# Performance work log

Hardware: AMD Instinct MI355X
Metric: run time of the kernel (lower is better)

Reference implementation:

```python
import jax, jax.numpy as jnp
import numpy as np

NUM_USERS, NUM_ITEMS, NUM_GROUPS = 100000, 50000, 20000
D = 64
B, M = 16384, 50


def setup_inputs() -> dict:
    key = jax.random.key(0)
    ks = jax.random.split(key, 16)
    inp = {
        "group_inputs": jax.random.randint(ks[0], (B,), 0, NUM_GROUPS),
        "item_inputs": jax.random.randint(ks[1], (B,), 0, NUM_ITEMS),
        "member_ids": jax.random.randint(ks[2], (B, M), 0, NUM_USERS),
        "member_lengths": jax.random.randint(ks[3], (B,), 0, M),
        # embedding tables (xavier-ish scale)
        "user_table": jax.random.normal(ks[4], (NUM_USERS, D), jnp.float32) * 0.05,
        "item_table": jax.random.normal(ks[5], (NUM_ITEMS, D), jnp.float32) * 0.05,
        "group_table": jax.random.normal(ks[6], (NUM_GROUPS, D), jnp.float32) * 0.05,
        # attention MLP: 2D -> 16 -> 1
        "att_w1": jax.random.normal(ks[7], (2 * D, 16), jnp.float32) * 0.1,
        "att_b1": jnp.zeros((16,), jnp.float32),
        "att_w2": jax.random.normal(ks[8], (16, 1), jnp.float32) * 0.1,
        "att_b2": jnp.zeros((1,), jnp.float32),
        # predict MLP: 3D -> 8 -> 1
        "pred_w1": jax.random.normal(ks[9], (3 * D, 8), jnp.float32) * 0.1,
        "pred_b1": jnp.zeros((8,), jnp.float32),
        "pred_w2": jax.random.normal(ks[10], (8, 1), jnp.float32) * 0.1,
        "pred_b2": jnp.zeros((1,), jnp.float32),
    }
    return inp


def reference(group_inputs, item_inputs, member_ids, member_lengths,
              user_table, item_table, group_table,
              att_w1, att_b1, att_w2, att_b2,
              pred_w1, pred_b1, pred_w2, pred_b2):
    # mask: at least one valid member per group
    mask = jnp.arange(M)[None, :] <= member_lengths[:, None]          # [B, M] bool
    mem_e = user_table[member_ids]                                    # [B, M, D]
    item_e = item_table[item_inputs]                                  # [B, D]

    # attention over members: concat(member, item) -> 16 -> 1
    gi = jnp.concatenate(
        [mem_e, jnp.broadcast_to(item_e[:, None, :], mem_e.shape)], axis=-1)  # [B, M, 2D]
    h = jax.nn.relu(jnp.einsum('bmk,kh->bmh', gi, att_w1) + att_b1)   # [B, M, 16]
    scores = (jnp.einsum('bmh,ho->bmo', h, att_w2) + att_b2)[..., 0]  # [B, M]
    scores = jnp.where(mask, scores, -jnp.inf)
    at_wt = jax.nn.softmax(scores, axis=-1)                           # [B, M]

    g_att = jnp.einsum('bm,bmd->bd', at_wt, mem_e)                    # [B, D]
    g = g_att + group_table[group_inputs]                             # [B, D]

    elem = g * item_e
    new_e = jnp.concatenate([elem, g, item_e], axis=-1)               # [B, 3D]
    ph = jax.nn.relu(new_e @ pred_w1 + pred_b1)                       # [B, 8]
    y = jax.nn.sigmoid(ph @ pred_w2 + pred_b2)                        # [B, 1]
    return y
```

## Files before the change

kernel.cpp:

```cpp
#include <hip/hip_runtime.h>
#include <math.h>

constexpr int MM = 50;
constexpr int DD = 64;
constexpr int HH = 16;
constexpr int PH = 8;
constexpr int WAVES_PER_BLOCK = 4;
constexpr int SLOTS  = 56;
constexpr int CHUNKS = 7;

__device__ __forceinline__ unsigned bf16rne(float f) {
    const unsigned u = __float_as_uint(f);
    return (u + 0x7FFFu + ((u >> 16) & 1u)) >> 16;
}

__global__ __launch_bounds__(256) void precompute_kernel(
    const float* __restrict__ user_table,
    const float* __restrict__ item_table,
    const int*   __restrict__ item_inputs,
    const float* __restrict__ att_w1,
    const float* __restrict__ att_b1,
    unsigned short* __restrict__ Ubf,
    float* __restrict__ Ib,
    unsigned short* __restrict__ Ub,
    int nU, int B, int userBlocks)
{
    const bool isU = (int)blockIdx.x < userBlocks;
    const float4* rp;
    const float*  w1;
    float acc[HH];
    int row = 0;

    if (isU) {
        row = (int)blockIdx.x * 256 + (int)threadIdx.x;
        if (row >= nU) return;
        rp  = (const float4*)(user_table + (size_t)row * DD);
        w1  = att_w1;
        #pragma unroll
        for (int j = 0; j < HH; ++j) acc[j] = 0.0f;
    } else {
        row = ((int)blockIdx.x - userBlocks) * 256 + (int)threadIdx.x;
        if (row >= B) return;
        const int item = item_inputs[row];
        rp  = (const float4*)(item_table + (size_t)item * DD);
        w1  = att_w1 + (size_t)DD * HH;
        #pragma unroll
        for (int j = 0; j < HH; ++j) acc[j] = att_b1[j];
    }

    unsigned brow[DD / 2];

    #pragma unroll 4
    for (int d4 = 0; d4 < DD / 4; ++d4) {
        const float4 x = rp[d4];
        const float* w = w1 + (size_t)(d4 * 4) * HH;
        #pragma unroll
        for (int j = 0; j < HH; ++j) {
            acc[j] = fmaf(x.x, w[0 * HH + j], acc[j]);
            acc[j] = fmaf(x.y, w[1 * HH + j], acc[j]);
            acc[j] = fmaf(x.z, w[2 * HH + j], acc[j]);
            acc[j] = fmaf(x.w, w[3 * HH + j], acc[j]);
        }
        brow[2 * d4]     = bf16rne(x.x) | (bf16rne(x.y) << 16);
        brow[2 * d4 + 1] = bf16rne(x.z) | (bf16rne(x.w) << 16);
    }

    if (isU) {
        unsigned uw[8];
        #pragma unroll
        for (int w = 0; w < 8; ++w)
            uw[w] = bf16rne(acc[2 * w]) | (bf16rne(acc[2 * w + 1]) << 16);
        uint4* u4 = (uint4*)(Ubf + (size_t)row * HH);
        u4[0] = make_uint4(uw[0], uw[1], uw[2], uw[3]);
        u4[1] = make_uint4(uw[4], uw[5], uw[6], uw[7]);

        uint4* b4 = (uint4*)(Ub + (size_t)row * DD);
        #pragma unroll
        for (int i = 0; i < DD / 8; ++i)
            b4[i] = make_uint4(brow[4 * i], brow[4 * i + 1],
                               brow[4 * i + 2], brow[4 * i + 3]);
    } else {
        float4* o4 = (float4*)(Ib + (size_t)row * HH);
        o4[0] = make_float4(acc[0],  acc[1],  acc[2],  acc[3]);
        o4[1] = make_float4(acc[4],  acc[5],  acc[6],  acc[7]);
        o4[2] = make_float4(acc[8],  acc[9],  acc[10], acc[11]);
        o4[3] = make_float4(acc[12], acc[13], acc[14], acc[15]);
    }
}

__global__ __launch_bounds__(256) void agree_main(
    const int* __restrict__ group_inputs,
    const int* __restrict__ item_inputs,
    const int* __restrict__ member_ids,
    const int* __restrict__ member_lengths,
    const float* __restrict__ item_table,
    const float* __restrict__ group_table,
    const float* __restrict__ att_w2,
    const float* __restrict__ att_b2,
    const float* __restrict__ pred_w1,
    const float* __restrict__ pred_b1,
    const float* __restrict__ pred_w2,
    const float* __restrict__ pred_b2,
    const unsigned short* __restrict__ Ubf,
    const float* __restrict__ Ib,
    const unsigned short* __restrict__ Ub,
    float* __restrict__ out,
    int B)
{
    __shared__ float2 pairs[WAVES_PER_BLOCK][SLOTS];
    __shared__ float  gbuf[WAVES_PER_BLOCK][DD];

    const int lane = threadIdx.x & 63;
    const int wv   = threadIdx.x >> 6;
    const int b    = blockIdx.x * WAVES_PER_BLOCK + wv;
    if (b >= B) return;

    const int my_m  = (lane < MM) ? lane : (MM - 1);
    const int my_id = member_ids[b * MM + my_m];
    const int len      = member_lengths[b];
    const int item_idx = item_inputs[b];
    const int gid      = group_inputs[b];

    const float item_d = item_table[(unsigned)(item_idx * DD + lane)];
    const float grp_d  = group_table[(unsigned)(gid * DD + lane)];

    const uint4* up = (const uint4*)(Ubf + ((size_t)(unsigned)my_id * HH));
    const uint4 ua = up[0], ubw = up[1];
    const float* ib = Ib + (size_t)b * HH;

    float score = att_b2[0];
    {
        const unsigned uw[8] = { ua.x, ua.y, ua.z, ua.w,
                                 ubw.x, ubw.y, ubw.z, ubw.w };
        #pragma unroll
        for (int w = 0; w < 8; ++w) {
            const float f0 = __uint_as_float(uw[w] << 16);
            const float f1 = __uint_as_float(uw[w] & 0xFFFF0000u);
            score = fmaf(fmaxf(f0 + ib[2 * w],     0.0f), att_w2[2 * w],     score);
            score = fmaf(fmaxf(f1 + ib[2 * w + 1], 0.0f), att_w2[2 * w + 1], score);
        }
    }

    const bool valid = (lane < MM) && (lane <= len);
    score = valid ? score : -INFINITY;

    float mx = score;
    #pragma unroll
    for (int off = 32; off > 0; off >>= 1) mx = fmaxf(mx, __shfl_xor(mx, off, 64));
    const float e = valid ? __expf(score - mx) : 0.0f;
    float sum = e;
    #pragma unroll
    for (int off = 32; off > 0; off >>= 1) sum += __shfl_xor(sum, off, 64);
    const float wnorm = e / sum;

    if (lane < SLOTS) pairs[wv][lane] = make_float2(wnorm, __int_as_float(my_id));
    __builtin_amdgcn_s_waitcnt(0);

    const int i = lane >> 3;
    const int j = lane & 7;

    float2 pr[CHUNKS];
    #pragma unroll
    for (int c = 0; c < CHUNKS; ++c) pr[c] = pairs[wv][c * 8 + i];

    uint4 r4[CHUNKS];
    #pragma unroll
    for (int c = 0; c < CHUNKS; ++c) {
        const unsigned row = (unsigned)__float_as_int(pr[c].y);
        r4[c] = *(const uint4*)(Ub + (size_t)row * DD + (j << 3));
    }

    float gp[8];
    #pragma unroll
    for (int r = 0; r < 8; ++r) gp[r] = 0.0f;
    #pragma unroll
    for (int c = 0; c < CHUNKS; ++c) {
        const float w = pr[c].x;
        const unsigned wd[4] = { r4[c].x, r4[c].y, r4[c].z, r4[c].w };
        #pragma unroll
        for (int t = 0; t < 4; ++t) {
            gp[2 * t]     = fmaf(w, __uint_as_float(wd[t] << 16),         gp[2 * t]);
            gp[2 * t + 1] = fmaf(w, __uint_as_float(wd[t] & 0xFFFF0000u), gp[2 * t + 1]);
        }
    }

    #pragma unroll
    for (int off = 8; off < 64; off <<= 1) {
        #pragma unroll
        for (int r = 0; r < 8; ++r) gp[r] += __shfl_xor(gp[r], off, 64);
    }

    if (lane < 8) {
        float4* g4 = (float4*)&gbuf[wv][lane * 8];
        g4[0] = make_float4(gp[0], gp[1], gp[2], gp[3]);
        g4[1] = make_float4(gp[4], gp[5], gp[6], gp[7]);
    }
    __builtin_amdgcn_s_waitcnt(0);

    const float g = gbuf[wv][lane] + grp_d;

    const float elem = g * item_d;
    float p[PH];
    {
        const float* pa = pred_w1 + (size_t)lane * PH;
        const float* pb = pred_w1 + (size_t)(DD + lane) * PH;
        const float* pc = pred_w1 + (size_t)(2 * DD + lane) * PH;
        #pragma unroll
        for (int jj = 0; jj < PH; ++jj)
            p[jj] = fmaf(elem, pa[jj], fmaf(g, pb[jj], item_d * pc[jj]));
    }
    #pragma unroll
    for (int off = 32; off > 0; off >>= 1) {
        #pragma unroll
        for (int jj = 0; jj < PH; ++jj) p[jj] += __shfl_xor(p[jj], off, 64);
    }

    if (lane == 0) {
        float acc = pred_b2[0];
        #pragma unroll
        for (int jj = 0; jj < PH; ++jj)
            acc = fmaf(fmaxf(p[jj] + pred_b1[jj], 0.0f), pred_w2[jj], acc);
        out[b] = 1.0f / (1.0f + __expf(-acc));
    }
}

__global__ __launch_bounds__(256) void agree_fallback(
    const int* __restrict__ group_inputs,
    const int* __restrict__ item_inputs,
    const int* __restrict__ member_ids,
    const int* __restrict__ member_lengths,
    const float* __restrict__ user_table,
    const float* __restrict__ item_table,
    const float* __restrict__ group_table,
    const float* __restrict__ att_w1,
    const float* __restrict__ att_b1,
    const float* __restrict__ att_w2,
    const float* __restrict__ att_b2,
    const float* __restrict__ pred_w1,
    const float* __restrict__ pred_b1,
    const float* __restrict__ pred_w2,
    const float* __restrict__ pred_b2,
    float* __restrict__ out,
    int B)
{
    __shared__ float lds_wt[4][MM];
    __shared__ int   lds_id[4][MM];

    const int lane = threadIdx.x & 63;
    const int wave = threadIdx.x >> 6;
    const int b = blockIdx.x * 4 + wave;
    if (b >= B) return;

    const int my_m = (lane < MM) ? lane : (MM - 1);
    const int my_id = member_ids[b * MM + my_m];
    if (lane < MM) lds_id[wave][lane] = my_id;

    const int item_idx = item_inputs[b];
    const float item_d = item_table[(size_t)item_idx * DD + lane];

    float h[HH];
    {
        const float* w1row = att_w1 + (size_t)(DD + lane) * HH;
        #pragma unroll
        for (int j = 0; j < HH; ++j) h[j] = item_d * w1row[j];
        #pragma unroll
        for (int off = 32; off > 0; off >>= 1) {
            #pragma unroll
            for (int j = 0; j < HH; ++j) h[j] += __shfl_xor(h[j], off, 64);
        }
        #pragma unroll
        for (int j = 0; j < HH; ++j) h[j] += att_b1[j];
    }

    const float* myrow = user_table + (size_t)my_id * DD;
    #pragma unroll 4
    for (int d4 = 0; d4 < DD / 4; ++d4) {
        const float4 x = ((const float4*)myrow)[d4];
        const float* w1d = att_w1 + (size_t)(d4 * 4) * HH;
        #pragma unroll
        for (int j = 0; j < HH; ++j) {
            h[j] = fmaf(x.x, w1d[0 * HH + j], h[j]);
            h[j] = fmaf(x.y, w1d[1 * HH + j], h[j]);
            h[j] = fmaf(x.z, w1d[2 * HH + j], h[j]);
            h[j] = fmaf(x.w, w1d[3 * HH + j], h[j]);
        }
    }

    float score = att_b2[0];
    #pragma unroll
    for (int j = 0; j < HH; ++j) score = fmaf(fmaxf(h[j], 0.0f), att_w2[j], score);

    const int len = member_lengths[b];
    const bool valid = (lane < MM) && (lane <= len);
    score = valid ? score : -INFINITY;

    float mx = score;
    #pragma unroll
    for (int off = 32; off > 0; off >>= 1) mx = fmaxf(mx, __shfl_xor(mx, off, 64));
    float e = valid ? __expf(score - mx) : 0.0f;
    float sum = e;
    #pragma unroll
    for (int off = 32; off > 0; off >>= 1) sum += __shfl_xor(sum, off, 64);
    if (lane < MM) lds_wt[wave][lane] = e / sum;
    __builtin_amdgcn_s_waitcnt(0);

    const int mcnt = (len < MM - 1 ? len : MM - 1) + 1;
    float g = 0.0f;
    #pragma unroll 2
    for (int m = 0; m < mcnt; ++m) {
        g = fmaf(lds_wt[wave][m],
                 user_table[(size_t)lds_id[wave][m] * DD + lane], g);
    }
    const int gid = group_inputs[b];
    g += group_table[(size_t)gid * DD + lane];

    const float elem = g * item_d;
    float p[PH];
    {
        const float* pa = pred_w1 + (size_t)lane * PH;
        const float* pb = pred_w1 + (size_t)(DD + lane) * PH;
        const float* pc = pred_w1 + (size_t)(2 * DD + lane) * PH;
        #pragma unroll
        for (int j = 0; j < PH; ++j)
            p[j] = fmaf(elem, pa[j], fmaf(g, pb[j], item_d * pc[j]));
    }
    #pragma unroll
    for (int off = 32; off > 0; off >>= 1) {
        #pragma unroll
        for (int j = 0; j < PH; ++j) p[j] += __shfl_xor(p[j], off, 64);
    }

    if (lane == 0) {
        float acc = pred_b2[0];
        #pragma unroll
        for (int j = 0; j < PH; ++j)
            acc = fmaf(fmaxf(p[j] + pred_b1[j], 0.0f), pred_w2[j], acc);
        out[b] = 1.0f / (1.0f + __expf(-acc));
    }
}

extern "C" void kernel_launch(void* const* d_in, const int* in_sizes, int n_in,
                              void* d_out, int out_size, void* d_ws, size_t ws_size,
                              hipStream_t stream) {
    const int*   group_inputs   = (const int*)d_in[0];
    const int*   item_inputs    = (const int*)d_in[1];
    const int*   member_ids     = (const int*)d_in[2];
    const int*   member_lengths = (const int*)d_in[3];
    const float* user_table     = (const float*)d_in[4];
    const float* item_table     = (const float*)d_in[5];
    const float* group_table    = (const float*)d_in[6];
    const float* att_w1         = (const float*)d_in[7];
    const float* att_b1         = (const float*)d_in[8];
    const float* att_w2         = (const float*)d_in[9];
    const float* att_b2         = (const float*)d_in[10];
    const float* pred_w1        = (const float*)d_in[11];
    const float* pred_b1        = (const float*)d_in[12];
    const float* pred_w2        = (const float*)d_in[13];
    const float* pred_b2        = (const float*)d_in[14];
    float* out = (float*)d_out;

    const int B  = in_sizes[0];
    const int nU = in_sizes[4] / DD;
    const size_t need = (size_t)nU * HH * sizeof(unsigned short)
                      + (size_t)B  * HH * sizeof(float)
                      + (size_t)nU * DD * sizeof(unsigned short);
    const int blocks = (B + WAVES_PER_BLOCK - 1) / WAVES_PER_BLOCK;

    if (ws_size >= need) {
        unsigned short* Ubf = (unsigned short*)d_ws;
        float* Ib = (float*)(Ubf + (size_t)nU * HH);
        unsigned short* Ub = (unsigned short*)(Ib + (size_t)B * HH);
        const int userBlocks = (nU + 255) / 256;
        const int itemBlocks = (B + 255) / 256;
        precompute_kernel<<<userBlocks + itemBlocks, 256, 0, stream>>>(
            user_table, item_table, item_inputs, att_w1, att_b1,
            Ubf, Ib, Ub, nU, B, userBlocks);
        agree_main<<<blocks, 256, 0, stream>>>(
            group_inputs, item_inputs, member_ids, member_lengths,
            item_table, group_table,
            att_w2, att_b2, pred_w1, pred_b1, pred_w2, pred_b2,
            Ubf, Ib, Ub, out, B);
    } else {
        agree_fallback<<<blocks, 256, 0, stream>>>(
            group_inputs, item_inputs, member_ids, member_lengths,
            user_table, item_table, group_table,
            att_w1, att_b1, att_w2, att_b2,
            pred_w1, pred_b1, pred_w2, pred_b2,
            out, B);
    }
}
```

Before: 144.5 us.

## Drop bf16 user table copy and gather only valid members from fp32 table

The precompute kernel no longer writes a bf16 copy of the whole user table, which removes about 12.8 MB of writes. The main kernel now gathers member rows straight from the fp32 user table, so each gather moves twice as many bytes. To offset that, it loops only over the chunks that contain valid members (based on member_lengths) instead of all 7 fixed chunks. The trade is less precompute traffic and fewer gathers against wider fp32 gathers and a loop with a data-dependent trip count.

```diff
diff --git a/kernel.cpp b/kernel.cpp
--- a/kernel.cpp
+++ b/kernel.cpp
@@ -7,7 +7,6 @@
 constexpr int PH = 8;
 constexpr int WAVES_PER_BLOCK = 4;
 constexpr int SLOTS  = 56;
-constexpr int CHUNKS = 7;
 
 __device__ __forceinline__ unsigned bf16rne(float f) {
     const unsigned u = __float_as_uint(f);
@@ -22,7 +21,6 @@
     const float* __restrict__ att_b1,
     unsigned short* __restrict__ Ubf,
     float* __restrict__ Ib,
-    unsigned short* __restrict__ Ub,
     int nU, int B, int userBlocks)
 {
     const bool isU = (int)blockIdx.x < userBlocks;
@@ -48,8 +46,6 @@
         for (int j = 0; j < HH; ++j) acc[j] = att_b1[j];
     }
 
-    unsigned brow[DD / 2];
-
     #pragma unroll 4
     for (int d4 = 0; d4 < DD / 4; ++d4) {
         const float4 x = rp[d4];
@@ -61,8 +57,6 @@
             acc[j] = fmaf(x.z, w[2 * HH + j], acc[j]);
             acc[j] = fmaf(x.w, w[3 * HH + j], acc[j]);
         }
-        brow[2 * d4]     = bf16rne(x.x) | (bf16rne(x.y) << 16);
-        brow[2 * d4 + 1] = bf16rne(x.z) | (bf16rne(x.w) << 16);
     }
 
     if (isU) {
@@ -73,12 +67,6 @@
         uint4* u4 = (uint4*)(Ubf + (size_t)row * HH);
         u4[0] = make_uint4(uw[0], uw[1], uw[2], uw[3]);
         u4[1] = make_uint4(uw[4], uw[5], uw[6], uw[7]);
-
-        uint4* b4 = (uint4*)(Ub + (size_t)row * DD);
-        #pragma unroll
-        for (int i = 0; i < DD / 8; ++i)
-            b4[i] = make_uint4(brow[4 * i], brow[4 * i + 1],
-                               brow[4 * i + 2], brow[4 * i + 3]);
     } else {
         float4* o4 = (float4*)(Ib + (size_t)row * HH);
         o4[0] = make_float4(acc[0],  acc[1],  acc[2],  acc[3]);
@@ -93,6 +81,7 @@
     const int* __restrict__ item_inputs,
     const int* __restrict__ member_ids,
     const int* __restrict__ member_lengths,
+    const float* __restrict__ user_table,
     const float* __restrict__ item_table,
     const float* __restrict__ group_table,
     const float* __restrict__ att_w2,
@@ -103,7 +92,6 @@
     const float* __restrict__ pred_b2,
     const unsigned short* __restrict__ Ubf,
     const float* __restrict__ Ib,
-    const unsigned short* __restrict__ Ub,
     float* __restrict__ out,
     int B)
 {
@@ -159,29 +147,26 @@
     const int i = lane >> 3;
     const int j = lane & 7;
 
-    float2 pr[CHUNKS];
-    #pragma unroll
-    for (int c = 0; c < CHUNKS; ++c) pr[c] = pairs[wv][c * 8 + i];
-
-    uint4 r4[CHUNKS];
-    #pragma unroll
-    for (int c = 0; c < CHUNKS; ++c) {
-        const unsigned row = (unsigned)__float_as_int(pr[c].y);
-        r4[c] = *(const uint4*)(Ub + (size_t)row * DD + (j << 3));
-    }
+    const int mcnt   = (len < MM - 1 ? len : MM - 1) + 1;
+    const int chunks = (mcnt + 7) >> 3;
 
     float gp[8];
     #pragma unroll
     for (int r = 0; r < 8; ++r) gp[r] = 0.0f;
-    #pragma unroll
-    for (int c = 0; c < CHUNKS; ++c) {
-        const float w = pr[c].x;
-        const unsigned wd[4] = { r4[c].x, r4[c].y, r4[c].z, r4[c].w };
-        #pragma unroll
-        for (int t = 0; t < 4; ++t) {
-            gp[2 * t]     = fmaf(w, __uint_as_float(wd[t] << 16),         gp[2 * t]);
-            gp[2 * t + 1] = fmaf(w, __uint_as_float(wd[t] & 0xFFFF0000u), gp[2 * t + 1]);
-        }
+
+    #pragma unroll 2
+    for (int c = 0; c < chunks; ++c) {
+        const float2 pr = pairs[wv][c * 8 + i];
+        const float4* rp =
+            (const float4*)(user_table
+                + (size_t)(unsigned)__float_as_int(pr.y) * DD + (j << 3));
+        const float4 a = rp[0];
+        const float4 d = rp[1];
+        const float w = pr.x;
+        gp[0] = fmaf(w, a.x, gp[0]);  gp[1] = fmaf(w, a.y, gp[1]);
+        gp[2] = fmaf(w, a.z, gp[2]);  gp[3] = fmaf(w, a.w, gp[3]);
+        gp[4] = fmaf(w, d.x, gp[4]);  gp[5] = fmaf(w, d.y, gp[5]);
+        gp[6] = fmaf(w, d.z, gp[6]);  gp[7] = fmaf(w, d.w, gp[7]);
     }
 
     #pragma unroll
@@ -362,24 +347,22 @@
     const int B  = in_sizes[0];
     const int nU = in_sizes[4] / DD;
     const size_t need = (size_t)nU * HH * sizeof(unsigned short)
-                      + (size_t)B  * HH * sizeof(float)
-                      + (size_t)nU * DD * sizeof(unsigned short);
+                      + (size_t)B  * HH * sizeof(float);
     const int blocks = (B + WAVES_PER_BLOCK - 1) / WAVES_PER_BLOCK;
 
     if (ws_size >= need) {
         unsigned short* Ubf = (unsigned short*)d_ws;
         float* Ib = (float*)(Ubf + (size_t)nU * HH);
-        unsigned short* Ub = (unsigned short*)(Ib + (size_t)B * HH);
         const int userBlocks = (nU + 255) / 256;
         const int itemBlocks = (B + 255) / 256;
         precompute_kernel<<<userBlocks + itemBlocks, 256, 0, stream>>>(
             user_table, item_table, item_inputs, att_w1, att_b1,
-            Ubf, Ib, Ub, nU, B, userBlocks);
+            Ubf, Ib, nU, B, userBlocks);
         agree_main<<<blocks, 256, 0, stream>>>(
             group_inputs, item_inputs, member_ids, member_lengths,
-            item_table, group_table,
+            user_table, item_table, group_table,
             att_w2, att_b2, pred_w1, pred_b1, pred_w2, pred_b2,
-            Ubf, Ib, Ub, out, B);
+            Ubf, Ib, out, B);
     } else {
         agree_fallback<<<blocks, 256, 0, stream>>>(
             group_inputs, item_inputs, member_ids, member_lengths,
```

Result: no change. 144.8 us (+0.2%).
